# Optimization experiments

Hardware: AMD Instinct MI355X
Metric: run time of the kernel (lower is better)

## Reference

```python
import jax, jax.numpy as jnp
import numpy as np


def setup_inputs() -> dict:
    key = jax.random.key(0)
    k1, k2 = jax.random.split(key)
    B, S, V = 256, 4096, 128000
    input_ids = jax.random.randint(k1, (B, S), 0, V, dtype=jnp.int32)
    last_token_index = jax.random.randint(k2, (B, 1), 0, S, dtype=jnp.int32)
    return {"input_ids": input_ids, "last_token_index": last_token_index, "vocab_size": V}


def reference(input_ids, last_token_index, vocab_size):
    # token_count[b, v] = #{ s : s < last_token_index[b] and input_ids[b, s] == v }
    B, S = input_ids.shape
    # positions >= last_token_index are invalid: remap to vocab_size (out of range -> dropped)
    valid = jnp.arange(S, dtype=jnp.int32)[None, :] < last_token_index  # (B, S)
    used_tokens = jnp.where(valid, input_ids, jnp.int32(vocab_size))    # (B, S)
    token_count = jnp.zeros((B, vocab_size), dtype=jnp.int32)
    # batched scatter-add histogram; out-of-range index vocab_size is dropped
    token_count = token_count.at[jnp.arange(B, dtype=jnp.int32)[:, None], used_tokens].add(
        jnp.int32(1), mode="drop")
    return token_count
```

## Files before the change

### kernel.cpp

```cpp
#include <hip/hip_runtime.h>


#define NB      256
#define SLEN    4096
#define VOC     128000
#define THREADS 256
#define BLOCKS_PER_ROW 16
#define BINS    8000
#define WORDS   (BINS / 2)
#define NXCD    8
#define TOK_VEC 4

typedef int vint4 __attribute__((ext_vector_type(4)));

__global__ __launch_bounds__(THREADS) void fused_hist_kernel(
    const int* __restrict__ input_ids,
    const int* __restrict__ last_token_index,
    int* __restrict__ out)
{
    __shared__ int lds[WORDS];

    const int i    = blockIdx.x;
    const int xcd  = i & (NXCD - 1);
    const int j    = i >> 3;
    const int b    = xcd * (NB / NXCD) + (j >> 4);
    const int part = j & (BLOCKS_PER_ROW - 1);
    const int lo   = part * BINS;

    const int* __restrict__ row_in = input_ids + (size_t)b * SLEN;
    int* __restrict__ row_out      = out + (size_t)b * VOC + lo;

    const int L = last_token_index[b];

    vint4 t[TOK_VEC];
#pragma unroll
    for (int k = 0; k < TOK_VEC; ++k) {
        const int v4 = threadIdx.x + k * THREADS;
        const int s0 = v4 * 4;
        vint4 w = { 0x40000000, 0x40000000, 0x40000000, 0x40000000 };
        if (s0 < L) {
            w = reinterpret_cast<const vint4*>(row_in)[v4];
            if (s0 + 1 >= L) w.y = 0x40000000;
            if (s0 + 2 >= L) w.z = 0x40000000;
            if (s0 + 3 >= L) w.w = 0x40000000;
        }
        t[k] = w;
    }

    {
        vint4 z = { 0, 0, 0, 0 };
        vint4* __restrict__ l4 = reinterpret_cast<vint4*>(lds);
        for (int k = threadIdx.x; k < WORDS / 4; k += THREADS) {
            l4[k] = z;
        }
    }
    __syncthreads();

#pragma unroll
    for (int k = 0; k < TOK_VEC; ++k) {
        const int tok[4] = { t[k].x, t[k].y, t[k].z, t[k].w };
#pragma unroll
        for (int e = 0; e < 4; ++e) {
            const unsigned d = (unsigned)(tok[e] - lo);
            if (d < (unsigned)BINS) {
                atomicAdd(&lds[d >> 1], 1 << ((d & 1) * 16));
            }
        }
    }
    __syncthreads();

    const int2* __restrict__ src = reinterpret_cast<const int2*>(lds);
    vint4* __restrict__ dst = reinterpret_cast<vint4*>(row_out);
    for (int k = threadIdx.x; k < BINS / 4; k += THREADS) {
        int2 w = src[k];
        vint4 o;
        o.x = w.x & 0xFFFF;
        o.y = (int)((unsigned)w.x >> 16);
        o.z = w.y & 0xFFFF;
        o.w = (int)((unsigned)w.y >> 16);
        dst[k] = o;
    }
}

extern "C" void kernel_launch(void* const* d_in, const int* in_sizes, int n_in,
                              void* d_out, int out_size, void* d_ws, size_t ws_size,
                              hipStream_t stream) {
    const int* input_ids        = (const int*)d_in[0];
    const int* last_token_index = (const int*)d_in[1];
    int* out = (int*)d_out;

    fused_hist_kernel<<<dim3(NB * BLOCKS_PER_ROW), dim3(THREADS), 0, stream>>>(
        input_ids, last_token_index, out);
}
```

Baseline: 24.87 us.

## Process four histogram partitions per block in two LDS sub-passes

Reduces the grid from 4096 to 1024 blocks of 512 threads. Each block covers a quarter of a row's vocabulary in two sequential 16000-bin LDS passes, reusing the tokens held in registers. This cuts the redundant re-reads of each input row and the per-block fixed overhead. In exchange it uses more LDS per block and adds serialization (zero, accumulate, write, repeat) inside each block.

```diff
diff --git a/kernel.cpp b/kernel.cpp
--- a/kernel.cpp
+++ b/kernel.cpp
@@ -4,12 +4,10 @@
 #define NB      256
 #define SLEN    4096
 #define VOC     128000
-#define THREADS 256
-#define BLOCKS_PER_ROW 16
-#define BINS    8000
-#define WORDS   (BINS / 2)
+#define THREADS 512
+#define PART_BINS   16000
+#define WORDS   (PART_BINS/2)
 #define NXCD    8
-#define TOK_VEC 4
 
 typedef int vint4 __attribute__((ext_vector_type(4)));
 
@@ -23,18 +21,17 @@
     const int i    = blockIdx.x;
     const int xcd  = i & (NXCD - 1);
     const int j    = i >> 3;
-    const int b    = xcd * (NB / NXCD) + (j >> 4);
-    const int part = j & (BLOCKS_PER_ROW - 1);
-    const int lo   = part * BINS;
+    const int b    = xcd * (NB / NXCD) + (j >> 2);
+    const int q    = j & 3;
 
     const int* __restrict__ row_in = input_ids + (size_t)b * SLEN;
-    int* __restrict__ row_out      = out + (size_t)b * VOC + lo;
+    int* __restrict__ out_row      = out + (size_t)b * VOC;
 
     const int L = last_token_index[b];
 
-    vint4 t[TOK_VEC];
+    vint4 t[2];
 #pragma unroll
-    for (int k = 0; k < TOK_VEC; ++k) {
+    for (int k = 0; k < 2; ++k) {
         const int v4 = threadIdx.x + k * THREADS;
         const int s0 = v4 * 4;
         vint4 w = { 0x40000000, 0x40000000, 0x40000000, 0x40000000 };
@@ -47,38 +44,47 @@
         t[k] = w;
     }
 
-    {
-        vint4 z = { 0, 0, 0, 0 };
-        vint4* __restrict__ l4 = reinterpret_cast<vint4*>(lds);
-        for (int k = threadIdx.x; k < WORDS / 4; k += THREADS) {
-            l4[k] = z;
+#pragma unroll
+    for (int sp = 0; sp < 2; ++sp) {
+        const int part = 2 * q + sp;
+        const int lo   = part * PART_BINS;
+
+        {
+            vint4 z = { 0, 0, 0, 0 };
+            vint4* __restrict__ l4 = reinterpret_cast<vint4*>(lds);
+            for (int k = threadIdx.x; k < WORDS / 4; k += THREADS) {
+                l4[k] = z;
+            }
         }
-    }
-    __syncthreads();
+        __syncthreads();
 
 #pragma unroll
-    for (int k = 0; k < TOK_VEC; ++k) {
-        const int tok[4] = { t[k].x, t[k].y, t[k].z, t[k].w };
+        for (int k = 0; k < 2; ++k) {
+            const int tok[4] = { t[k].x, t[k].y, t[k].z, t[k].w };
 #pragma unroll
-        for (int e = 0; e < 4; ++e) {
-            const unsigned d = (unsigned)(tok[e] - lo);
-            if (d < (unsigned)BINS) {
-                atomicAdd(&lds[d >> 1], 1 << ((d & 1) * 16));
+            for (int e = 0; e < 4; ++e) {
+                const unsigned d = (unsigned)(tok[e] - lo);
+                if (d < (unsigned)PART_BINS) {
+                    atomicAdd(&lds[d >> 1], 1 << ((d & 1) * 16));
+                }
             }
         }
-    }
-    __syncthreads();
+        __syncthreads();
 
-    const int2* __restrict__ src = reinterpret_cast<const int2*>(lds);
-    vint4* __restrict__ dst = reinterpret_cast<vint4*>(row_out);
-    for (int k = threadIdx.x; k < BINS / 4; k += THREADS) {
-        int2 w = src[k];
-        vint4 o;
-        o.x = w.x & 0xFFFF;
-        o.y = (int)((unsigned)w.x >> 16);
-        o.z = w.y & 0xFFFF;
-        o.w = (int)((unsigned)w.y >> 16);
-        dst[k] = o;
+        {
+            const int2* __restrict__ src = reinterpret_cast<const int2*>(lds);
+            vint4* __restrict__ dst = reinterpret_cast<vint4*>(out_row + lo);
+            for (int k = threadIdx.x; k < PART_BINS / 4; k += THREADS) {
+                int2 w = src[k];
+                vint4 o;
+                o.x = w.x & 0xFFFF;
+                o.y = (int)((unsigned)w.x >> 16);
+                o.z = w.y & 0xFFFF;
+                o.w = (int)((unsigned)w.y >> 16);
+                dst[k] = o;
+            }
+        }
+        if (sp == 0) __syncthreads();
     }
 }
 
@@ -89,6 +95,6 @@
     const int* last_token_index = (const int*)d_in[1];
     int* out = (int*)d_out;
 
-    fused_hist_kernel<<<dim3(NB * BLOCKS_PER_ROW), dim3(THREADS), 0, stream>>>(
+    fused_hist_kernel<<<dim3(1024), dim3(THREADS), 0, stream>>>(
         input_ids, last_token_index, out);
 }
```

Result: faster. 24.13 us (-3.0%).
